# Optimization experiments

Hardware: AMD Instinct MI355X
Metric: run time of the kernel (lower is better)

Reference implementation:

```python
import jax, jax.numpy as jnp
import numpy as np

B, C, H, W = 4, 256, 64, 64
CQK = C // 2


def setup_inputs() -> dict:
    key = jax.random.key(0)
    ks = jax.random.split(key, 8)
    s = 0.05
    return {
        "x": jax.random.normal(ks[0], (B, C, H, W), dtype=jnp.float32),
        "wq": jax.random.normal(ks[1], (CQK, C), dtype=jnp.float32) * s,
        "bq": jax.random.normal(ks[2], (CQK,), dtype=jnp.float32) * s,
        "wk": jax.random.normal(ks[3], (CQK, C), dtype=jnp.float32) * s,
        "bk": jax.random.normal(ks[4], (CQK,), dtype=jnp.float32) * s,
        "wv": jax.random.normal(ks[5], (C, C), dtype=jnp.float32) * s,
        "bv": jax.random.normal(ks[6], (C,), dtype=jnp.float32) * s,
        "gamma": jax.random.normal(ks[7], (1,), dtype=jnp.float32),
    }


def reference(x, wq, bq, wk, bk, wv, bv, gamma):
    b, c, h, w = x.shape
    n = h * w
    xf = x.reshape(b, c, n)  # [B,C,N]
    # 1x1 convs == per-pixel linear projections
    q = jnp.einsum("oc,bcn->bon", wq, xf) + bq[:, None]  # [B,C/2,N]
    k = jnp.einsum("oc,bcn->bon", wk, xf) + bk[:, None]  # [B,C/2,N]
    v = jnp.einsum("oc,bcn->bon", wv, xf) + bv[:, None]  # [B,C,N]
    # attention[b,m,n'] = softmax_n'( sum_d q[b,d,m] * k[b,d,n'] )
    scores = jnp.einsum("bdm,bdn->bmn", q, k)  # [B,N,N]
    attn = jax.nn.softmax(scores, axis=2)
    # out_feat[b,c,j] = sum_i v[b,c,i] * attn[b,i,j]  (matmul(value, attention))
    af = jnp.einsum("bci,bij->bcj", v, attn)  # [B,C,N]
    out = gamma[0] * af.reshape(b, c, h, w) + x
    return out
```

## Files before the change

kernel.cpp:

```cpp
#include <hip/hip_runtime.h>
#include <hip/hip_bf16.h>


typedef _Float16 f16;
typedef _Float16 f16x4v __attribute__((ext_vector_type(4)));
typedef _Float16 f16x8v __attribute__((ext_vector_type(8)));
typedef float f32x4v __attribute__((ext_vector_type(4)));

static __device__ __forceinline__ f32x4v mfma16(f16x8v a, f16x8v b, f32x4v c) {
  return __builtin_amdgcn_mfma_f32_16x16x32_f16(a, b, c, 0, 0, 0);
}

__global__ void k_wcvt(const float* __restrict__ wq, const float* __restrict__ bq,
                       const float* __restrict__ wk, const float* __restrict__ bk,
                       const float* __restrict__ wv, const float* __restrict__ bv,
                       f16* __restrict__ wh, float* __restrict__ bcat) {
  int o = blockIdx.x;
  int c = threadIdx.x;
  const float* wrow; float bias;
  if (o < 128)      { wrow = wq + (size_t)o * 256;         bias = bq[o]; }
  else if (o < 256) { wrow = wk + (size_t)(o - 128) * 256; bias = bk[o - 128]; }
  else              { wrow = wv + (size_t)(o - 256) * 256; bias = bv[o - 256]; }
  wh[(size_t)(o >> 4) * 4096 + (size_t)(c >> 5) * 512 +
     (size_t)((c >> 3) & 3) * 128 + (o & 15) * 8 + (c & 7)] = (f16)wrow[c];
  if (c == 0) bcat[o] = bias;
}

__global__ void k_xsplit(const float* __restrict__ x, f16* __restrict__ xh) {
  __shared__ float t[64][65];
  int b = blockIdx.z, c0 = blockIdx.y * 64, n0 = blockIdx.x * 64;
  int tx = threadIdx.x & 63, ty = threadIdx.x >> 6;
  const float* xb = x + ((size_t)b * 256 + c0) * 4096 + n0;
#pragma unroll
  for (int r = ty; r < 64; r += 4) t[r][tx] = xb[(size_t)r * 4096 + tx];
  __syncthreads();
  f16* xbb = xh + (size_t)b * 1048576;
#pragma unroll
  for (int k2 = 0; k2 < 2; k2++) {
    int id = k2 * 256 + threadIdx.x;
    int tok = id & 63, oct = id >> 6;
    int tt = n0 + tok;
    f16x8v v;
#pragma unroll
    for (int e = 0; e < 8; e++) v[e] = (f16)t[oct * 8 + e][tok];
    size_t addr = (size_t)(tt >> 4) * 4096 +
                  (size_t)((c0 >> 5) + (oct >> 2)) * 512 +
                  (size_t)(oct & 3) * 128 + (tt & 15) * 8;
    *(f16x8v*)&xbb[addr] = v;
  }
}

__global__ void __launch_bounds__(512, 1)
k_proj(const f16* __restrict__ xh, const f16* __restrict__ wh,
       const float* __restrict__ bcat, f16* __restrict__ qT,
       f16* __restrict__ kT, f16* __restrict__ vT) {
  int ob = blockIdx.x, th = blockIdx.y, b = blockIdx.z;
  int tid = threadIdx.x, l = tid & 63, w = tid >> 6;
  int col = l & 15, quad = l >> 4;
  int tt = w & 3, oh = w >> 2;
  int OT0 = ob * 4 + oh * 2;
  const f16* wtb = wh + (size_t)OT0 * 4096 + l * 8;
  f16x8v wb[2][8];
#pragma unroll
  for (int jt = 0; jt < 2; jt++)
#pragma unroll
    for (int ks = 0; ks < 8; ks++)
      wb[jt][ks] = *(const f16x8v*)(wtb + jt * 4096 + ks * 512);
  float bias0 = bcat[OT0 * 16 + col];
  float bias1 = bcat[OT0 * 16 + 16 + col];
  const f16* atb = xh + (size_t)b * 1048576 + (size_t)(th * 32 + tt) * 4096 + l * 8;
  f16x8v afA[8], afB[8];
#pragma unroll
  for (int ks = 0; ks < 8; ks++) afA[ks] = *(const f16x8v*)(atb + ks * 512);

#define PROJ_BODY(IT, AF, AN, PREF)                                            \
  {                                                                            \
    if (PREF) {                                                                \
      _Pragma("unroll") for (int ks = 0; ks < 8; ks++)                         \
        AN[ks] = *(const f16x8v*)(atb + (size_t)((IT) + 1) * 16384 + ks * 512);\
    }                                                                          \
    f32x4v s0 = {}, s1 = {};                                                   \
    _Pragma("unroll") for (int ks = 0; ks < 8; ks++) {                         \
      s0 = mfma16(AF[ks], wb[0][ks], s0);                                      \
      s1 = mfma16(AF[ks], wb[1][ks], s1);                                      \
    }                                                                          \
    int T = th * 32 + (IT) * 4 + tt;                                           \
    if (ob < 4) {                                                              \
      f16* dst = (ob < 2) ? qT : kT;                                           \
      _Pragma("unroll") for (int jt = 0; jt < 2; jt++) {                       \
        int o = OT0 * 16 + jt * 16 + col;                                      \
        int d = o & 127;                                                       \
        float bs = jt ? bias1 : bias0;                                         \
        size_t base = (size_t)b * 524288 + (size_t)T * 2048 +                  \
                      (size_t)(d >> 5) * 512 + (size_t)((d >> 3) & 3) * 128 +  \
                      (d & 7);                                                 \
        float sv0 = jt ? s1[0] : s0[0], sv1 = jt ? s1[1] : s0[1];              \
        float sv2 = jt ? s1[2] : s0[2], sv3 = jt ? s1[3] : s0[3];              \
        dst[base + (quad * 4 + 0) * 8] = (f16)(sv0 + bs);                      \
        dst[base + (quad * 4 + 1) * 8] = (f16)(sv1 + bs);                      \
        dst[base + (quad * 4 + 2) * 8] = (f16)(sv2 + bs);                      \
        dst[base + (quad * 4 + 3) * 8] = (f16)(sv3 + bs);                      \
      }                                                                        \
    } else {                                                                   \
      int i0 = T * 16 + quad * 4;                                              \
      size_t ibase = (size_t)b * 1048576 + (size_t)(i0 >> 5) * 512 +           \
                     (size_t)((i0 >> 3) & 3) * 128 + (i0 & 7);                 \
      _Pragma("unroll") for (int jt = 0; jt < 2; jt++) {                       \
        int c = OT0 * 16 + jt * 16 + col - 256;                                \
        float bs = jt ? bias1 : bias0;                                         \
        f16x4v pv;                                                             \
        _Pragma("unroll") for (int rg = 0; rg < 4; rg++)                       \
          pv[rg] = (f16)((jt ? s1[rg] : s0[rg]) + bs);                         \
        *(f16x4v*)&vT[ibase + (size_t)(c >> 4) * 65536 + (c & 15) * 8] = pv;   \
      }                                                                        \
    }                                                                          \
  }

  for (int itp = 0; itp < 4; itp++) {
    int itA = itp * 2;
    PROJ_BODY(itA, afA, afB, true)
    PROJ_BODY(itA + 1, afB, afA, itp < 3)
  }
#undef PROJ_BODY
}

__global__ void __launch_bounds__(512, 2)
k_rows(const f16* __restrict__ qT, const f16* __restrict__ kT,
       float* __restrict__ partial) {
  int jblk = blockIdx.x, ih = blockIdx.y, b = blockIdx.z;
  int tid = threadIdx.x, l = tid & 63, w = tid >> 6;
  int col = l & 15;
  int ti = w & 3, jh = w >> 2;
  const f16* ktb = kT + (size_t)b * 524288 + (size_t)(jblk * 8 + jh * 4) * 2048 + l * 8;
  const f16* qtb = qT + (size_t)b * 524288 + (size_t)ti * 2048 + l * 8;
  f16x8v ka[4][4];
#pragma unroll
  for (int jt = 0; jt < 4; jt++)
#pragma unroll
    for (int ks = 0; ks < 4; ks++)
      ka[jt][ks] = *(const f16x8v*)(ktb + jt * 2048 + ks * 512);
  float* pout = partial + ((size_t)(b * 32 + jblk) * 2 + jh) * 4096 + ti * 16 + col;
  int it0 = ih * 32;
  f16x8v qfA[4], qfB[4];
#pragma unroll
  for (int ks = 0; ks < 4; ks++)
    qfA[ks] = *(const f16x8v*)(qtb + (size_t)it0 * 8192 + ks * 512);

#define ROWS_BODY(IT, QF, QN, PREF)                                           \
  {                                                                           \
    if (PREF) {                                                               \
      _Pragma("unroll") for (int ks = 0; ks < 4; ks++)                        \
        QN[ks] = *(const f16x8v*)(qtb + (size_t)((IT) + 1) * 8192 + ks * 512);\
    }                                                                         \
    f32x4v s[4] = {};                                                         \
    _Pragma("unroll") for (int ks = 0; ks < 4; ks++) {                        \
      s[0] = mfma16(ka[0][ks], QF[ks], s[0]);                                 \
      s[1] = mfma16(ka[1][ks], QF[ks], s[1]);                                 \
      s[2] = mfma16(ka[2][ks], QF[ks], s[2]);                                 \
      s[3] = mfma16(ka[3][ks], QF[ks], s[3]);                                 \
    }                                                                         \
    float t = 0.f;                                                            \
    _Pragma("unroll") for (int jt = 0; jt < 4; jt++)                          \
      _Pragma("unroll") for (int rg = 0; rg < 4; rg++)                        \
        t += __expf(s[jt][rg]);                                               \
    t += __shfl_xor(t, 16);                                                   \
    t += __shfl_xor(t, 32);                                                   \
    if (l < 16) pout[(size_t)(IT) * 64] = t;                                  \
  }

  for (int itp = 0; itp < 16; itp++) {
    int itA = it0 + itp * 2;
    ROWS_BODY(itA, qfA, qfB, true)
    ROWS_BODY(itA + 1, qfB, qfA, itp < 15)
  }
#undef ROWS_BODY
}

__global__ void k_rsum(const float* __restrict__ partial, float* __restrict__ rinv) {
  int b = blockIdx.y;
  int i = blockIdx.x * 256 + threadIdx.x;
  const float* p = partial + (size_t)b * 64 * 4096 + i;
  float s = 0.f;
#pragma unroll 8
  for (int jb = 0; jb < 64; jb++) s += p[(size_t)jb * 4096];
  rinv[(size_t)b * 4096 + i] = 1.0f / s;
}

__global__ void __launch_bounds__(512, 2)
k_fav(const f16* __restrict__ qT, const f16* __restrict__ kT,
      const f16* __restrict__ vT, const float* __restrict__ rinv,
      const float* __restrict__ x, const float* __restrict__ gamma,
      float* __restrict__ out) {
  __shared__ f16 sE[2][4096];
  int wg = blockIdx.x;
  int lg = (wg & 7) * 32 + (wg >> 3);
  int b = lg >> 6, j0 = (lg & 63) * 64;
  int tid = threadIdx.x, l = tid & 63, w = tid >> 6;
  int col = l & 15, quad = l >> 4;
  int ti = w & 3, tjb = (w >> 2) * 2;
  const f16* ktb = kT + (size_t)b * 524288 + (size_t)(j0 / 16 + tjb) * 2048 + l * 8;
  const f16* qtb = qT + (size_t)b * 524288 + (size_t)ti * 2048 + l * 8;
  const f16* vtb = vT + (size_t)b * 1048576 + (size_t)(w * 2) * 65536 + l * 8;
  const float* rp = rinv + (size_t)b * 4096 + ti * 16 + col;
  f16x8v ka0[4], ka1[4];
#pragma unroll
  for (int ks = 0; ks < 4; ks++) {
    ka0[ks] = *(const f16x8v*)(ktb + ks * 512);
    ka1[ks] = *(const f16x8v*)(ktb + 2048 + ks * 512);
  }
  f16x8v qfA[4], qfB[4], vfA[2][2], vfB[2][2];
  float rvA, rvB;
#pragma unroll
  for (int ks = 0; ks < 4; ks++) qfA[ks] = *(const f16x8v*)(qtb + ks * 512);
#pragma unroll
  for (int mt = 0; mt < 2; mt++)
#pragma unroll
    for (int ks = 0; ks < 2; ks++)
      vfA[mt][ks] = *(const f16x8v*)(vtb + mt * 65536 + ks * 512);
  rvA = rp[0];
  f32x4v acc[2][4] = {};
  int ig = ti * 2 + (col >> 3);
  int i_lo = col & 7;

#define FAV_BODY(IT, QF, VF, RV, QN, VN, RN, PREF, SEB)                        \
  {                                                                            \
    if (PREF) {                                                                \
      _Pragma("unroll") for (int ks = 0; ks < 4; ks++)                         \
        QN[ks] = *(const f16x8v*)(qtb + (size_t)((IT) + 1) * 8192 + ks * 512); \
      _Pragma("unroll") for (int mt = 0; mt < 2; mt++)                         \
        _Pragma("unroll") for (int ks = 0; ks < 2; ks++)                       \
          VN[mt][ks] = *(const f16x8v*)(vtb + mt * 65536 +                     \
                                        (size_t)(((IT) + 1) * 2 + ks) * 512);  \
      RN = rp[((IT) + 1) * 64];                                                \
    }                                                                          \
    f32x4v s0 = {}, s1 = {};                                                   \
    _Pragma("unroll") for (int ks = 0; ks < 4; ks++) {                         \
      s0 = mfma16(ka0[ks], QF[ks], s0);                                        \
      s1 = mfma16(ka1[ks], QF[ks], s1);                                        \
    }                                                                          \
    _Pragma("unroll") for (int rg = 0; rg < 4; rg++) {                         \
      int jl0 = tjb * 16 + quad * 4 + rg;                                      \
      sE[SEB][jl0 * 64 + ((ig ^ (jl0 & 7)) * 8) + i_lo] = (f16)(__expf(s0[rg]) * RV); \
      sE[SEB][(jl0 + 16) * 64 + ((ig ^ (jl0 & 7)) * 8) + i_lo] = (f16)(__expf(s1[rg]) * RV); \
    }                                                                          \
    asm volatile("s_waitcnt lgkmcnt(0)\n\ts_barrier" ::: "memory");            \
    _Pragma("unroll") for (int ks = 0; ks < 2; ks++) {                         \
      int sw = ((ks * 4 + quad) ^ (col & 7)) * 8;                              \
      f16x8v e0 = *(const f16x8v*)&sE[SEB][col * 64 + sw];                     \
      f16x8v e1 = *(const f16x8v*)&sE[SEB][(16 + col) * 64 + sw];              \
      f16x8v e2 = *(const f16x8v*)&sE[SEB][(32 + col) * 64 + sw];              \
      f16x8v e3 = *(const f16x8v*)&sE[SEB][(48 + col) * 64 + sw];              \
      acc[0][0] = mfma16(VF[0][ks], e0, acc[0][0]);                            \
      acc[0][1] = mfma16(VF[0][ks], e1, acc[0][1]);                            \
      acc[0][2] = mfma16(VF[0][ks], e2, acc[0][2]);                            \
      acc[0][3] = mfma16(VF[0][ks], e3, acc[0][3]);                            \
      acc[1][0] = mfma16(VF[1][ks], e0, acc[1][0]);                            \
      acc[1][1] = mfma16(VF[1][ks], e1, acc[1][1]);                            \
      acc[1][2] = mfma16(VF[1][ks], e2, acc[1][2]);                            \
      acc[1][3] = mfma16(VF[1][ks], e3, acc[1][3]);                            \
    }                                                                          \
  }

  for (int itp = 0; itp < 32; itp++) {
    int itA = itp * 2;
    FAV_BODY(itA, qfA, vfA, rvA, qfB, vfB, rvB, true, 0)
    FAV_BODY(itA + 1, qfB, vfB, rvB, qfA, vfA, rvA, itp < 31, 1)
  }
#undef FAV_BODY

  float gm = gamma[0];
  const float* xb = x + (size_t)b * 256 * 4096;
  float* ob = out + (size_t)b * 256 * 4096;
#pragma unroll
  for (int mt = 0; mt < 2; mt++)
#pragma unroll
    for (int jt = 0; jt < 4; jt++) {
      int c = w * 32 + mt * 16 + quad * 4;
      int j = j0 + jt * 16 + col;
#pragma unroll
      for (int rg = 0; rg < 4; rg++) {
        size_t off = (size_t)(c + rg) * 4096 + j;
        ob[off] = gm * acc[mt][jt][rg] + xb[off];
      }
    }
}

extern "C" void kernel_launch(void* const* d_in, const int* in_sizes, int n_in,
                              void* d_out, int out_size, void* d_ws, size_t ws_size,
                              hipStream_t stream) {
  (void)in_sizes; (void)n_in; (void)out_size; (void)ws_size;
  const float* x  = (const float*)d_in[0];
  const float* wq = (const float*)d_in[1];
  const float* bq = (const float*)d_in[2];
  const float* wk = (const float*)d_in[3];
  const float* bk = (const float*)d_in[4];
  const float* wv = (const float*)d_in[5];
  const float* bv = (const float*)d_in[6];
  const float* gm = (const float*)d_in[7];
  float* out = (float*)d_out;

  char* ws = (char*)d_ws;
  f16*  xh = (f16*)ws;
  f16*  qT = (f16*)(ws + 8388608);
  f16*  kT = (f16*)(ws + 12582912);
  f16*  vT = (f16*)(ws + 16777216);
  f16*  wh = (f16*)(ws + 25165824);
  float* bcat    = (float*)(ws + 25427968);
  float* rinv    = (float*)(ws + 25430016);
  float* partial = (float*)(ws + 25495552);

  hipLaunchKernelGGL(k_wcvt, dim3(512), dim3(256), 0, stream, wq, bq, wk, bk, wv, bv, wh, bcat);
  hipLaunchKernelGGL(k_xsplit, dim3(64, 4, 4), dim3(256), 0, stream, x, xh);
  hipLaunchKernelGGL(k_proj, dim3(8, 8, 4), dim3(512), 0, stream, xh, wh, bcat, qT, kT, vT);
  hipLaunchKernelGGL(k_rows, dim3(32, 2, 4), dim3(512), 0, stream, qT, kT, partial);
  hipLaunchKernelGGL(k_rsum, dim3(16, 4), dim3(256), 0, stream, partial, rinv);
  hipLaunchKernelGGL(k_fav, dim3(256), dim3(512), 0, stream, qT, kT, vT, rinv, x, gm, out);
}
```

Before: 178.4 us.

## Split k_fav output channels across two workgroups to double grid size

The attention-times-V kernel now launches 512 workgroups instead of 256. Each workgroup handles half of the 256 output channels (128) for a 64-column tile, and each wave keeps one 16-channel V tile instead of two. This raises the number of workgroups available to the 256 CUs and lowers per-thread register and accumulator use. The cost is that the QK^T scores and exp are computed twice, once for each channel half, and Q and K are read twice.

```diff
diff --git a/kernel.cpp b/kernel.cpp
--- a/kernel.cpp
+++ b/kernel.cpp
@@ -193,14 +193,17 @@
       float* __restrict__ out) {
   __shared__ f16 sE[2][4096];
   int wg = blockIdx.x;
-  int lg = (wg & 7) * 32 + (wg >> 3);
-  int b = lg >> 6, j0 = (lg & 63) * 64;
+  int lg = (wg & 7) * 64 + (wg >> 3);
+  int b = lg >> 7;
+  int rem = lg & 127;
+  int j0 = (rem >> 1) * 64;
+  int ch = rem & 1;
   int tid = threadIdx.x, l = tid & 63, w = tid >> 6;
   int col = l & 15, quad = l >> 4;
   int ti = w & 3, tjb = (w >> 2) * 2;
   const f16* ktb = kT + (size_t)b * 524288 + (size_t)(j0 / 16 + tjb) * 2048 + l * 8;
   const f16* qtb = qT + (size_t)b * 524288 + (size_t)ti * 2048 + l * 8;
-  const f16* vtb = vT + (size_t)b * 1048576 + (size_t)(w * 2) * 65536 + l * 8;
+  const f16* vtb = vT + (size_t)b * 1048576 + (size_t)(ch * 8 + w) * 65536 + l * 8;
   const float* rp = rinv + (size_t)b * 4096 + ti * 16 + col;
   f16x8v ka0[4], ka1[4];
 #pragma unroll
@@ -208,17 +211,15 @@
     ka0[ks] = *(const f16x8v*)(ktb + ks * 512);
     ka1[ks] = *(const f16x8v*)(ktb + 2048 + ks * 512);
   }
-  f16x8v qfA[4], qfB[4], vfA[2][2], vfB[2][2];
+  f16x8v qfA[4], qfB[4], vfA[2], vfB[2];
   float rvA, rvB;
 #pragma unroll
   for (int ks = 0; ks < 4; ks++) qfA[ks] = *(const f16x8v*)(qtb + ks * 512);
 #pragma unroll
-  for (int mt = 0; mt < 2; mt++)
-#pragma unroll
-    for (int ks = 0; ks < 2; ks++)
-      vfA[mt][ks] = *(const f16x8v*)(vtb + mt * 65536 + ks * 512);
+  for (int ks = 0; ks < 2; ks++)
+    vfA[ks] = *(const f16x8v*)(vtb + ks * 512);
   rvA = rp[0];
-  f32x4v acc[2][4] = {};
+  f32x4v acc[4] = {};
   int ig = ti * 2 + (col >> 3);
   int i_lo = col & 7;
 
@@ -227,10 +228,8 @@
     if (PREF) {                                                                \
       _Pragma("unroll") for (int ks = 0; ks < 4; ks++)                         \
         QN[ks] = *(const f16x8v*)(qtb + (size_t)((IT) + 1) * 8192 + ks * 512); \
-      _Pragma("unroll") for (int mt = 0; mt < 2; mt++)                         \
-        _Pragma("unroll") for (int ks = 0; ks < 2; ks++)                       \
-          VN[mt][ks] = *(const f16x8v*)(vtb + mt * 65536 +                     \
-                                        (size_t)(((IT) + 1) * 2 + ks) * 512);  \
+      _Pragma("unroll") for (int ks = 0; ks < 2; ks++)                         \
+        VN[ks] = *(const f16x8v*)(vtb + (size_t)(((IT) + 1) * 2 + ks) * 512);  \
       RN = rp[((IT) + 1) * 64];                                                \
     }                                                                          \
     f32x4v s0 = {}, s1 = {};                                                   \
@@ -250,14 +249,10 @@
       f16x8v e1 = *(const f16x8v*)&sE[SEB][(16 + col) * 64 + sw];              \
       f16x8v e2 = *(const f16x8v*)&sE[SEB][(32 + col) * 64 + sw];              \
       f16x8v e3 = *(const f16x8v*)&sE[SEB][(48 + col) * 64 + sw];              \
-      acc[0][0] = mfma16(VF[0][ks], e0, acc[0][0]);                            \
-      acc[0][1] = mfma16(VF[0][ks], e1, acc[0][1]);                            \
-      acc[0][2] = mfma16(VF[0][ks], e2, acc[0][2]);                            \
-      acc[0][3] = mfma16(VF[0][ks], e3, acc[0][3]);                            \
-      acc[1][0] = mfma16(VF[1][ks], e0, acc[1][0]);                            \
-      acc[1][1] = mfma16(VF[1][ks], e1, acc[1][1]);                            \
-      acc[1][2] = mfma16(VF[1][ks], e2, acc[1][2]);                            \
-      acc[1][3] = mfma16(VF[1][ks], e3, acc[1][3]);                            \
+      acc[0] = mfma16(VF[ks], e0, acc[0]);                                     \
+      acc[1] = mfma16(VF[ks], e1, acc[1]);                                     \
+      acc[2] = mfma16(VF[ks], e2, acc[2]);                                     \
+      acc[3] = mfma16(VF[ks], e3, acc[3]);                                     \
     }                                                                          \
   }
 
@@ -272,17 +267,15 @@
   const float* xb = x + (size_t)b * 256 * 4096;
   float* ob = out + (size_t)b * 256 * 4096;
 #pragma unroll
-  for (int mt = 0; mt < 2; mt++)
-#pragma unroll
-    for (int jt = 0; jt < 4; jt++) {
-      int c = w * 32 + mt * 16 + quad * 4;
-      int j = j0 + jt * 16 + col;
-#pragma unroll
-      for (int rg = 0; rg < 4; rg++) {
-        size_t off = (size_t)(c + rg) * 4096 + j;
-        ob[off] = gm * acc[mt][jt][rg] + xb[off];
-      }
+  for (int jt = 0; jt < 4; jt++) {
+    int c = ch * 128 + w * 16 + quad * 4;
+    int j = j0 + jt * 16 + col;
+#pragma unroll
+    for (int rg = 0; rg < 4; rg++) {
+      size_t off = (size_t)(c + rg) * 4096 + j;
+      ob[off] = gm * acc[jt][rg] + xb[off];
     }
+  }
 }
 
 extern "C" void kernel_launch(void* const* d_in, const int* in_sizes, int n_in,
@@ -314,5 +307,5 @@
   hipLaunchKernelGGL(k_proj, dim3(8, 8, 4), dim3(512), 0, stream, xh, wh, bcat, qT, kT, vT);
   hipLaunchKernelGGL(k_rows, dim3(32, 2, 4), dim3(512), 0, stream, qT, kT, partial);
   hipLaunchKernelGGL(k_rsum, dim3(16, 4), dim3(256), 0, stream, partial, rinv);
-  hipLaunchKernelGGL(k_fav, dim3(256), dim3(512), 0, stream, qT, kT, vT, rinv, x, gm, out);
-}
+  hipLaunchKernelGGL(k_fav, dim3(512), dim3(512), 0, stream, qT, kT, vT, rinv, x, gm, out);
+}
```

Measured after the change: 198.4 us. 11.2% more time.

## Process two key tiles per barrier in fused attention kernel and split row-sum grid

Applied to the files above, without the earlier changes.

The attention-times-value kernel now computes exp-scores for two i-tiles into a double-buffered, parity-indexed shared array before one barrier, instead of one barrier per tile. This halves the number of workgroup barriers. Next Q tiles and row scales are loaded after the barrier, and V tiles are loaded at the start of each step. Launch bounds drop to one block per CU, freeing registers for the larger live set. Separately, the row-sum kernel's grid doubles along the i dimension, so each block covers half as many rows, which adds parallelism.

```diff
diff --git a/kernel.cpp b/kernel.cpp
--- a/kernel.cpp
+++ b/kernel.cpp
@@ -140,7 +140,7 @@
     for (int ks = 0; ks < 4; ks++)
       ka[jt][ks] = *(const f16x8v*)(ktb + jt * 2048 + ks * 512);
   float* pout = partial + ((size_t)(b * 32 + jblk) * 2 + jh) * 4096 + ti * 16 + col;
-  int it0 = ih * 32;
+  int it0 = ih * 16;
   f16x8v qfA[4], qfB[4];
 #pragma unroll
   for (int ks = 0; ks < 4; ks++)
@@ -168,10 +168,10 @@
     if (l < 16) pout[(size_t)(IT) * 64] = t;                                  \
   }
 
-  for (int itp = 0; itp < 16; itp++) {
+  for (int itp = 0; itp < 8; itp++) {
     int itA = it0 + itp * 2;
     ROWS_BODY(itA, qfA, qfB, true)
-    ROWS_BODY(itA + 1, qfB, qfA, itp < 15)
+    ROWS_BODY(itA + 1, qfB, qfA, itp < 7)
   }
 #undef ROWS_BODY
 }
@@ -186,12 +186,12 @@
   rinv[(size_t)b * 4096 + i] = 1.0f / s;
 }
 
-__global__ void __launch_bounds__(512, 2)
+__global__ void __launch_bounds__(512, 1)
 k_fav(const f16* __restrict__ qT, const f16* __restrict__ kT,
       const f16* __restrict__ vT, const float* __restrict__ rinv,
       const float* __restrict__ x, const float* __restrict__ gamma,
       float* __restrict__ out) {
-  __shared__ f16 sE[2][4096];
+  __shared__ f16 sE[2][2][4096];
   int wg = blockIdx.x;
   int lg = (wg & 7) * 32 + (wg >> 3);
   int b = lg >> 6, j0 = (lg & 63) * 64;
@@ -211,28 +211,18 @@
   f16x8v qfA[4], qfB[4], vfA[2][2], vfB[2][2];
   float rvA, rvB;
 #pragma unroll
-  for (int ks = 0; ks < 4; ks++) qfA[ks] = *(const f16x8v*)(qtb + ks * 512);
-#pragma unroll
-  for (int mt = 0; mt < 2; mt++)
-#pragma unroll
-    for (int ks = 0; ks < 2; ks++)
-      vfA[mt][ks] = *(const f16x8v*)(vtb + mt * 65536 + ks * 512);
+  for (int ks = 0; ks < 4; ks++) {
+    qfA[ks] = *(const f16x8v*)(qtb + ks * 512);
+    qfB[ks] = *(const f16x8v*)(qtb + 8192 + ks * 512);
+  }
   rvA = rp[0];
+  rvB = rp[64];
   f32x4v acc[2][4] = {};
   int ig = ti * 2 + (col >> 3);
   int i_lo = col & 7;
 
-#define FAV_BODY(IT, QF, VF, RV, QN, VN, RN, PREF, SEB)                        \
+#define FAV_QK(QF, RV, SEP, SET)                                               \
   {                                                                            \
-    if (PREF) {                                                                \
-      _Pragma("unroll") for (int ks = 0; ks < 4; ks++)                         \
-        QN[ks] = *(const f16x8v*)(qtb + (size_t)((IT) + 1) * 8192 + ks * 512); \
-      _Pragma("unroll") for (int mt = 0; mt < 2; mt++)                         \
-        _Pragma("unroll") for (int ks = 0; ks < 2; ks++)                       \
-          VN[mt][ks] = *(const f16x8v*)(vtb + mt * 65536 +                     \
-                                        (size_t)(((IT) + 1) * 2 + ks) * 512);  \
-      RN = rp[((IT) + 1) * 64];                                                \
-    }                                                                          \
     f32x4v s0 = {}, s1 = {};                                                   \
     _Pragma("unroll") for (int ks = 0; ks < 4; ks++) {                         \
       s0 = mfma16(ka0[ks], QF[ks], s0);                                        \
@@ -240,16 +230,21 @@
     }                                                                          \
     _Pragma("unroll") for (int rg = 0; rg < 4; rg++) {                         \
       int jl0 = tjb * 16 + quad * 4 + rg;                                      \
-      sE[SEB][jl0 * 64 + ((ig ^ (jl0 & 7)) * 8) + i_lo] = (f16)(__expf(s0[rg]) * RV); \
-      sE[SEB][(jl0 + 16) * 64 + ((ig ^ (jl0 & 7)) * 8) + i_lo] = (f16)(__expf(s1[rg]) * RV); \
-    }                                                                          \
-    asm volatile("s_waitcnt lgkmcnt(0)\n\ts_barrier" ::: "memory");            \
+      sE[SEP][SET][jl0 * 64 + ((ig ^ (jl0 & 7)) * 8) + i_lo] =                 \
+          (f16)(__expf(s0[rg]) * RV);                                          \
+      sE[SEP][SET][(jl0 + 16) * 64 + ((ig ^ (jl0 & 7)) * 8) + i_lo] =          \
+          (f16)(__expf(s1[rg]) * RV);                                          \
+    }                                                                          \
+  }
+
+#define FAV_AV(VF, SEP, SET)                                                   \
+  {                                                                            \
     _Pragma("unroll") for (int ks = 0; ks < 2; ks++) {                         \
       int sw = ((ks * 4 + quad) ^ (col & 7)) * 8;                              \
-      f16x8v e0 = *(const f16x8v*)&sE[SEB][col * 64 + sw];                     \
-      f16x8v e1 = *(const f16x8v*)&sE[SEB][(16 + col) * 64 + sw];              \
-      f16x8v e2 = *(const f16x8v*)&sE[SEB][(32 + col) * 64 + sw];              \
-      f16x8v e3 = *(const f16x8v*)&sE[SEB][(48 + col) * 64 + sw];              \
+      f16x8v e0 = *(const f16x8v*)&sE[SEP][SET][col * 64 + sw];                \
+      f16x8v e1 = *(const f16x8v*)&sE[SEP][SET][(16 + col) * 64 + sw];         \
+      f16x8v e2 = *(const f16x8v*)&sE[SEP][SET][(32 + col) * 64 + sw];         \
+      f16x8v e3 = *(const f16x8v*)&sE[SEP][SET][(48 + col) * 64 + sw];         \
       acc[0][0] = mfma16(VF[0][ks], e0, acc[0][0]);                            \
       acc[0][1] = mfma16(VF[0][ks], e1, acc[0][1]);                            \
       acc[0][2] = mfma16(VF[0][ks], e2, acc[0][2]);                            \
@@ -261,12 +256,33 @@
     }                                                                          \
   }
 
-  for (int itp = 0; itp < 32; itp++) {
-    int itA = itp * 2;
-    FAV_BODY(itA, qfA, vfA, rvA, qfB, vfB, rvB, true, 0)
-    FAV_BODY(itA + 1, qfB, vfB, rvB, qfA, vfA, rvA, itp < 31, 1)
-  }
-#undef FAV_BODY
+  for (int s = 0; s < 32; s++) {
+    int t0 = s * 2;
+    int p = s & 1;
+#pragma unroll
+    for (int mt = 0; mt < 2; mt++)
+#pragma unroll
+      for (int ks = 0; ks < 2; ks++) {
+        vfA[mt][ks] = *(const f16x8v*)(vtb + mt * 65536 + (size_t)(t0 * 2 + ks) * 512);
+        vfB[mt][ks] = *(const f16x8v*)(vtb + mt * 65536 + (size_t)(t0 * 2 + 2 + ks) * 512);
+      }
+    if (p) { FAV_QK(qfA, rvA, 1, 0) FAV_QK(qfB, rvB, 1, 1) }
+    else   { FAV_QK(qfA, rvA, 0, 0) FAV_QK(qfB, rvB, 0, 1) }
+    asm volatile("s_waitcnt lgkmcnt(0)\n\ts_barrier" ::: "memory");
+    if (s < 31) {
+#pragma unroll
+      for (int ks = 0; ks < 4; ks++) {
+        qfA[ks] = *(const f16x8v*)(qtb + (size_t)(t0 + 2) * 8192 + ks * 512);
+        qfB[ks] = *(const f16x8v*)(qtb + (size_t)(t0 + 3) * 8192 + ks * 512);
+      }
+      rvA = rp[(size_t)(t0 + 2) * 64];
+      rvB = rp[(size_t)(t0 + 3) * 64];
+    }
+    if (p) { FAV_AV(vfA, 1, 0) FAV_AV(vfB, 1, 1) }
+    else   { FAV_AV(vfA, 0, 0) FAV_AV(vfB, 0, 1) }
+  }
+#undef FAV_QK
+#undef FAV_AV
 
   float gm = gamma[0];
   const float* xb = x + (size_t)b * 256 * 4096;
@@ -312,7 +328,7 @@
   hipLaunchKernelGGL(k_wcvt, dim3(512), dim3(256), 0, stream, wq, bq, wk, bk, wv, bv, wh, bcat);
   hipLaunchKernelGGL(k_xsplit, dim3(64, 4, 4), dim3(256), 0, stream, x, xh);
   hipLaunchKernelGGL(k_proj, dim3(8, 8, 4), dim3(512), 0, stream, xh, wh, bcat, qT, kT, vT);
-  hipLaunchKernelGGL(k_rows, dim3(32, 2, 4), dim3(512), 0, stream, qT, kT, partial);
+  hipLaunchKernelGGL(k_rows, dim3(32, 4, 4), dim3(512), 0, stream, qT, kT, partial);
   hipLaunchKernelGGL(k_rsum, dim3(16, 4), dim3(256), 0, stream, partial, rinv);
   hipLaunchKernelGGL(k_fav, dim3(256), dim3(512), 0, stream, qT, kT, vT, rinv, x, gm, out);
 }
```

Measured after the change: 180.9 us. Within noise of the previous version (+1.4%).
